# Performance work log

Measured on AMD Instinct MI355X. Metric: run time of the kernel, lower is better.

Reference implementation:

```python
import jax, jax.numpy as jnp
import numpy as np


def setup_inputs() -> dict:
    key = jax.random.key(0)
    ks = jax.random.split(key, 7)
    B, S, D = 32, 1024, 1024
    R = 5
    return {
        "x": jax.random.normal(ks[0], (B, S, D), dtype=jnp.float32),
        "W": jax.random.normal(ks[1], (3 * D, D), dtype=jnp.float32) * 0.02,
        "bias": jax.random.normal(ks[2], (3 * D,), dtype=jnp.float32) * 0.02,
        "A0": jax.random.normal(ks[3], (R, D), dtype=jnp.float32) * 0.02,
        "A1": jax.random.normal(ks[4], (R, D), dtype=jnp.float32) * 0.02,
        "B0": jax.random.normal(ks[5], (D, R), dtype=jnp.float32) * 0.02,
        "B1": jax.random.normal(ks[6], (D, R), dtype=jnp.float32) * 0.02,
        "s0": jnp.ones((), dtype=jnp.float32),
        "s1": jnp.ones((), dtype=jnp.float32),
    }


def reference(x, W, bias, A0, A1, B0, B1, s0, s1):
    # weight delta: [2*out, in] = cat(s0*(B0@A0), s1*(B1@A1)), zero-padded
    # at the top to match W's rows (LoRA on K,V of a fused QKV projection).
    delta_kv = jnp.concatenate([s0 * (B0 @ A0), s1 * (B1 @ A1)], axis=0)  # [2D, D]
    pad_rows = W.shape[0] - delta_kv.shape[0]
    delta = jnp.concatenate(
        [jnp.zeros((pad_rows, W.shape[1]), dtype=W.dtype), delta_kv], axis=0
    )  # [3D, D]
    # F.linear: x @ (W + delta)^T + bias
    return jnp.einsum("bsd,od->bso", x, W + delta) + bias
```

## Files before the change

kernel.cpp:

```cpp
#include <hip/hip_runtime.h>
#include <stdint.h>

#define D_DIM 1024
#define M_DIM 32768
#define N_DIM 3072
#define K_DIM 1024
#define R_DIM 5

#define BM 256
#define BN 256
#define BK 64
#define NKT (K_DIM / BK)

typedef __bf16 bf16x8 __attribute__((ext_vector_type(8)));
typedef float  f32x4  __attribute__((ext_vector_type(4)));
typedef unsigned short ushort8 __attribute__((ext_vector_type(8)));

#define GLOBAL_AS(p) ((const __attribute__((address_space(1))) void*)(p))
#define LDS_AS(p)    ((__attribute__((address_space(3))) void*)(p))

__device__ __forceinline__ unsigned short f2bf(float f) {
    union { float f; unsigned int u; } v; v.f = f;
    unsigned int u = v.u;
    return (unsigned short)((u + 0x7fffu + ((u >> 16) & 1u)) >> 16);
}

__global__ __launch_bounds__(256) void build_weff_kernel(
    const float* __restrict__ W,
    const float* __restrict__ A0, const float* __restrict__ A1,
    const float* __restrict__ B0, const float* __restrict__ B1,
    const float* __restrict__ s0p, const float* __restrict__ s1p,
    unsigned short* __restrict__ Weff)
{
    int idx = blockIdx.x * blockDim.x + threadIdx.x;
    int o = idx >> 10;
    int c = idx & 1023;
    float w = W[idx];
    if (o >= D_DIM) {
        if (o < 2 * D_DIM) {
            const float* b = B0 + (long)(o - D_DIM) * R_DIM;
            float d = b[0] * A0[c]             + b[1] * A0[D_DIM + c]
                    + b[2] * A0[2 * D_DIM + c] + b[3] * A0[3 * D_DIM + c]
                    + b[4] * A0[4 * D_DIM + c];
            w += s0p[0] * d;
        } else {
            const float* b = B1 + (long)(o - 2 * D_DIM) * R_DIM;
            float d = b[0] * A1[c]             + b[1] * A1[D_DIM + c]
                    + b[2] * A1[2 * D_DIM + c] + b[3] * A1[3 * D_DIM + c]
                    + b[4] * A1[4 * D_DIM + c];
            w += s1p[0] * d;
        }
    }
    Weff[idx] = f2bf(w);
}

__global__ __launch_bounds__(256) void cvt_x_kernel(
    const float* __restrict__ x, unsigned short* __restrict__ xb)
{
    long idx = (long)blockIdx.x * blockDim.x + threadIdx.x;
    const f32x4* xv = (const f32x4*)x;
    f32x4 a = xv[2 * idx];
    f32x4 b = xv[2 * idx + 1];
    ushort8 r;
    r[0] = f2bf(a[0]); r[1] = f2bf(a[1]); r[2] = f2bf(a[2]); r[3] = f2bf(a[3]);
    r[4] = f2bf(b[0]); r[5] = f2bf(b[1]); r[6] = f2bf(b[2]); r[7] = f2bf(b[3]);
    *(ushort8*)(xb + 8 * idx) = r;
}

__global__ __launch_bounds__(512, 2) void gemm_kernel(
    const unsigned short* __restrict__ A,
    const unsigned short* __restrict__ Bw,
    const float* __restrict__ bias,
    float* __restrict__ C)
{
    __shared__ __align__(16) unsigned short lds[2][2][BM * BK];

    const int tid  = threadIdx.x;
    const int lane = tid & 63;
    const int wave = tid >> 6;
    const int wm   = wave >> 2;
    const int wnq  = wave & 3;
    const int r16  = lane & 15;
    const int quad = lane >> 4;

    const int nwg = (M_DIM / BM) * (N_DIM / BN);
    const int cpx = nwg / 8;
    int bid = blockIdx.x;
    bid = (bid % 8) * cpx + (bid / 8);
    const int m0 = (bid / (N_DIM / BN)) * BM;
    const int n0 = (bid % (N_DIM / BN)) * BN;

    const int jrow  = tid >> 3;
    const int chunk = (tid & 7) ^ (jrow & 7);
    const unsigned short* aG = A  + (long)(m0 + jrow) * K_DIM + chunk * 8;
    const unsigned short* bG = Bw + (long)(n0 + jrow) * K_DIM + chunk * 8;

#define STAGE(b, t) do {                                                        \
    const unsigned short* _as = aG + (t) * BK;                                  \
    const unsigned short* _bs = bG + (t) * BK;                                  \
    unsigned short* _al = &lds[b][0][0] + tid * 8;                              \
    unsigned short* _bl = &lds[b][1][0] + tid * 8;                              \
    _Pragma("unroll")                                                           \
    for (int j = 0; j < 4; ++j) {                                               \
        __builtin_amdgcn_global_load_lds(GLOBAL_AS(_as + (long)j * 64 * K_DIM), \
                                         LDS_AS(_al + j * 4096), 16, 0, 0);     \
        __builtin_amdgcn_global_load_lds(GLOBAL_AS(_bs + (long)j * 64 * K_DIM), \
                                         LDS_AS(_bl + j * 4096), 16, 0, 0);     \
    }                                                                           \
} while (0)

#define BARRIER() do { asm volatile("" ::: "memory");                 \
                       __builtin_amdgcn_s_barrier();                  \
                       asm volatile("" ::: "memory"); } while (0)
#define VMCNT(n) asm volatile("s_waitcnt vmcnt(" #n ")" ::: "memory")

    int sA[2];
    sA[0] = ((0 * 4 + quad) ^ (r16 & 7)) * 8;
    sA[1] = ((1 * 4 + quad) ^ (r16 & 7)) * 8;
    const int arowbase = (wm * 128 + r16) * BK;
    const int browbase = (wnq * 64 + r16) * BK;

#define LDA(b, mt, kk) (*(const bf16x8*)(&lds[b][0][0] + arowbase + (mt) * 16 * BK + sA[kk]))
#define LDB(b, nt, kk) (*(const bf16x8*)(&lds[b][1][0] + browbase + (nt) * 16 * BK + sA[kk]))

    bf16x8 af[4][2];
    bf16x8 bf[4][2];
    f32x4  acc[8][4] = {};

#define PHASE_LDA(b, msub)                                  \
    _Pragma("unroll")                                       \
    for (int m = 0; m < 4; ++m) {                           \
        af[m][0] = LDA(b, (msub) * 4 + m, 0);               \
        af[m][1] = LDA(b, (msub) * 4 + m, 1);               \
    }
#define PHASE_LDB(b, nsub)                                  \
    _Pragma("unroll")                                       \
    for (int n = 0; n < 2; ++n) {                           \
        bf[(nsub) * 2 + n][0] = LDB(b, (nsub) * 2 + n, 0);  \
        bf[(nsub) * 2 + n][1] = LDB(b, (nsub) * 2 + n, 1);  \
    }

#define MFMA_QUAD(ms, ns) do {                                                   \
    __builtin_amdgcn_s_setprio(1);                                               \
    _Pragma("unroll")                                                            \
    for (int m = 0; m < 4; ++m)                                                  \
    _Pragma("unroll")                                                            \
    for (int n = 0; n < 2; ++n)                                                  \
    _Pragma("unroll")                                                            \
    for (int kk = 0; kk < 2; ++kk)                                               \
        acc[(ms) * 4 + m][(ns) * 2 + n] = __builtin_amdgcn_mfma_f32_16x16x32_bf16( \
            af[m][kk], bf[(ns) * 2 + n][kk], acc[(ms) * 4 + m][(ns) * 2 + n], 0, 0, 0); \
    __builtin_amdgcn_s_setprio(0);                                               \
} while (0)

#define KTILE(b, tnext, dostage) do {                       \
    PHASE_LDA(b, 0); PHASE_LDB(b, 0);                       \
    BARRIER(); MFMA_QUAD(0, 0); BARRIER();                  \
    PHASE_LDB(b, 1);                                        \
    BARRIER(); MFMA_QUAD(0, 1); BARRIER();                  \
    PHASE_LDA(b, 1);                                        \
    BARRIER(); MFMA_QUAD(1, 0); BARRIER();                  \
    if (dostage) { STAGE(b, tnext); VMCNT(8); }             \
    else         { VMCNT(0); }                              \
    BARRIER(); MFMA_QUAD(1, 1); BARRIER();                  \
} while (0)

    STAGE(0, 0);
    STAGE(1, 1);
    VMCNT(8);
    BARRIER();

    for (int i = 0; i < NKT / 2; ++i) {
        const bool st = (i < NKT / 2 - 1);
        KTILE(0, 2 * i + 2, st);
        KTILE(1, 2 * i + 3, st);
    }

#pragma unroll
    for (int nt = 0; nt < 4; ++nt) {
        const int col = n0 + wnq * 64 + nt * 16 + r16;
        const float bv = bias[col];
#pragma unroll
        for (int mt = 0; mt < 8; ++mt) {
            const long row = m0 + wm * 128 + mt * 16 + quad * 4;
            float* Cp = C + row * (long)N_DIM + col;
#pragma unroll
            for (int r = 0; r < 4; ++r)
                Cp[(long)r * N_DIM] = acc[mt][nt][r] + bv;
        }
    }
}

extern "C" void kernel_launch(void* const* d_in, const int* in_sizes, int n_in,
                              void* d_out, int out_size, void* d_ws, size_t ws_size,
                              hipStream_t stream) {
    const float* x    = (const float*)d_in[0];
    const float* W    = (const float*)d_in[1];
    const float* bias = (const float*)d_in[2];
    const float* A0   = (const float*)d_in[3];
    const float* A1   = (const float*)d_in[4];
    const float* B0   = (const float*)d_in[5];
    const float* B1   = (const float*)d_in[6];
    const float* s0   = (const float*)d_in[7];
    const float* s1   = (const float*)d_in[8];
    float* out = (float*)d_out;

    unsigned short* Weff = (unsigned short*)d_ws;
    unsigned short* xb   = Weff + (size_t)N_DIM * K_DIM;

    build_weff_kernel<<<(N_DIM * K_DIM) / 256, 256, 0, stream>>>(
        W, A0, A1, B0, B1, s0, s1, Weff);

    cvt_x_kernel<<<((long)M_DIM * K_DIM) / (256 * 8), 256, 0, stream>>>(x, xb);

    dim3 grid((M_DIM / BM) * (N_DIM / BN));
    gemm_kernel<<<grid, 512, 0, stream>>>(xb, Weff, bias, out);
}
```

Measured before the change: 729.5 us.

## Split tile staging into quarter loads interleaved across GEMM phases

Global-to-LDS staging of each K tile is split into four quarter loads. Half of the next buffer's quarters are issued early, inside the current tile's first phases, and the rest are issued later, so memory traffic is spread across the MFMA phases. Explicit sched_barrier fences are added around barriers and waitcnts to pin the instruction order, and the main loop is no longer unrolled. This aims to overlap loads with compute more evenly, but it changes the buffer-reuse timing and vmcnt accounting, so a wrong count could cause a race.

```diff
diff --git a/kernel.cpp b/kernel.cpp
--- a/kernel.cpp
+++ b/kernel.cpp
@@ -95,24 +95,18 @@
     const unsigned short* aG = A  + (long)(m0 + jrow) * K_DIM + chunk * 8;
     const unsigned short* bG = Bw + (long)(n0 + jrow) * K_DIM + chunk * 8;
 
-#define STAGE(b, t) do {                                                        \
-    const unsigned short* _as = aG + (t) * BK;                                  \
-    const unsigned short* _bs = bG + (t) * BK;                                  \
-    unsigned short* _al = &lds[b][0][0] + tid * 8;                              \
-    unsigned short* _bl = &lds[b][1][0] + tid * 8;                              \
-    _Pragma("unroll")                                                           \
-    for (int j = 0; j < 4; ++j) {                                               \
-        __builtin_amdgcn_global_load_lds(GLOBAL_AS(_as + (long)j * 64 * K_DIM), \
-                                         LDS_AS(_al + j * 4096), 16, 0, 0);     \
-        __builtin_amdgcn_global_load_lds(GLOBAL_AS(_bs + (long)j * 64 * K_DIM), \
-                                         LDS_AS(_bl + j * 4096), 16, 0, 0);     \
-    }                                                                           \
+#define STAGE_J(b, t, j) do {                                                   \
+    __builtin_amdgcn_global_load_lds(                                           \
+        GLOBAL_AS(aG + (t) * BK + (long)(j) * 64 * K_DIM),                      \
+        LDS_AS(&lds[b][0][0] + tid * 8 + (j) * 4096), 16, 0, 0);                \
+    __builtin_amdgcn_global_load_lds(                                           \
+        GLOBAL_AS(bG + (t) * BK + (long)(j) * 64 * K_DIM),                      \
+        LDS_AS(&lds[b][1][0] + tid * 8 + (j) * 4096), 16, 0, 0);                \
 } while (0)
 
-#define BARRIER() do { asm volatile("" ::: "memory");                 \
-                       __builtin_amdgcn_s_barrier();                  \
-                       asm volatile("" ::: "memory"); } while (0)
-#define VMCNT(n) asm volatile("s_waitcnt vmcnt(" #n ")" ::: "memory")
+#define SCHEDB() __builtin_amdgcn_sched_barrier(0)
+#define BAR() do { SCHEDB(); __builtin_amdgcn_s_barrier(); SCHEDB(); } while (0)
+#define VMCNT(n) do { SCHEDB(); asm volatile("s_waitcnt vmcnt(" #n ")"); SCHEDB(); } while (0)
 
     int sA[2];
     sA[0] = ((0 * 4 + quad) ^ (r16 & 7)) * 8;
@@ -153,27 +147,36 @@
     __builtin_amdgcn_s_setprio(0);                                               \
 } while (0)
 
-#define KTILE(b, tnext, dostage) do {                       \
-    PHASE_LDA(b, 0); PHASE_LDB(b, 0);                       \
-    BARRIER(); MFMA_QUAD(0, 0); BARRIER();                  \
-    PHASE_LDB(b, 1);                                        \
-    BARRIER(); MFMA_QUAD(0, 1); BARRIER();                  \
-    PHASE_LDA(b, 1);                                        \
-    BARRIER(); MFMA_QUAD(1, 0); BARRIER();                  \
-    if (dostage) { STAGE(b, tnext); VMCNT(8); }             \
-    else         { VMCNT(0); }                              \
-    BARRIER(); MFMA_QUAD(1, 1); BARRIER();                  \
+#define HALF(rb, tE, stE, tL, stL, vmA) do {                \
+                                                    \
+    PHASE_LDB(rb, 0); PHASE_LDA(rb, 0);                     \
+    if (stE) STAGE_J((rb) ^ 1, tE, 2);                      \
+    BAR(); SCHEDB(); MFMA_QUAD(0, 0); SCHEDB(); BAR();      \
+                                                    \
+    PHASE_LDB(rb, 1);                                       \
+    if (stE) STAGE_J((rb) ^ 1, tE, 3);                      \
+    BAR(); SCHEDB(); MFMA_QUAD(0, 1); SCHEDB(); BAR();      \
+                                                    \
+    PHASE_LDA(rb, 1);                                       \
+    BAR(); SCHEDB(); MFMA_QUAD(1, 0); SCHEDB(); BAR();      \
+                                                    \
+    if (stL) { STAGE_J(rb, tL, 0); STAGE_J(rb, tL, 1); }    \
+    BAR(); SCHEDB(); MFMA_QUAD(1, 1); SCHEDB();             \
+    if (stL)      { VMCNT(4); }                             \
+    else if (vmA) { VMCNT(0); }                             \
+    BAR();                                                  \
 } while (0)
 
-    STAGE(0, 0);
-    STAGE(1, 1);
-    VMCNT(8);
-    BARRIER();
-
+    STAGE_J(0, 0, 0); STAGE_J(0, 0, 1); STAGE_J(0, 0, 2); STAGE_J(0, 0, 3);
+    STAGE_J(1, 1, 0); STAGE_J(1, 1, 1);
+    VMCNT(4);
+    BAR();
+
+#pragma unroll 1
     for (int i = 0; i < NKT / 2; ++i) {
         const bool st = (i < NKT / 2 - 1);
-        KTILE(0, 2 * i + 2, st);
-        KTILE(1, 2 * i + 3, st);
+        HALF(0, 2 * i + 1, true, 2 * i + 2, st, 1);
+        HALF(1, 2 * i + 2, st, 2 * i + 3, st, 0);
     }
 
 #pragma unroll
```

Result: no change. 717.5 us (-1.7%).
